# Performance work log

Hardware: AMD Instinct MI355X
Metric: run time of the kernel (lower is better)

Reference implementation:

```python
import jax, jax.numpy as jnp
import numpy as np

LEVELS = 32
RANGE = 1.0


def fake_quantize(w, levels=LEVELS, r=RANGE):
    # clamp -> scale -> round (straight-through) -> unscale
    wc = jnp.clip(w, -r, r)
    scale = (levels - 1) / (2 * r)
    ws = (wc + r) * scale
    wr = jax.lax.stop_gradient(jnp.round(ws) - ws) + ws  # STE round
    return wr / scale - r


def analog_linear(x, w, b):
    return x @ fake_quantize(w).T + b


def rnn_layer(x_seq, w_ih, w_hh, b_ih, b_hh):
    # x_seq: [B, T, I]; returns [B, T, H]. Plain tanh RNN, h0 = 0.
    B = x_seq.shape[0]
    H = w_hh.shape[0]
    # precompute input contribution once (memory-bound GEMM outside the scan)
    pre = jnp.einsum('bti,hi->bth', x_seq, w_ih) + b_ih + b_hh  # [B,T,H]
    pre_t = jnp.swapaxes(pre, 0, 1)  # [T,B,H]

    def step(h, p):
        h_new = jnp.tanh(p + h @ w_hh.T)
        return h_new, h_new

    h0 = jnp.zeros((B, H), dtype=x_seq.dtype)
    _, hs = jax.lax.scan(step, h0, pre_t)
    return jnp.swapaxes(hs, 0, 1)  # [B,T,H]


def setup_inputs() -> dict:
    key = jax.random.key(0)
    ks = jax.random.split(key, 20)
    B, T, F = 32, 8192, 10
    H, L = 256, 3
    CTX = F - 1  # 9
    RNN_IN = 1 + 32  # 33

    def init(k, shape, fan_in):
        bound = 1.0 / np.sqrt(fan_in)
        return jax.random.uniform(k, shape, jnp.float32, -bound, bound)

    inp = {
        'x': jax.random.normal(ks[0], (B, T, F), jnp.float32),
        # context MLP: 9 -> 64 -> 32
        'W1': init(ks[1], (64, CTX), CTX), 'b1': init(ks[2], (64,), CTX),
        'W2': init(ks[3], (32, 64), 64), 'b2': init(ks[4], (32,), 64),
        # RNN layers
        'w_ih0': init(ks[5], (H, RNN_IN), H), 'w_hh0': init(ks[6], (H, H), H),
        'b_ih0': init(ks[7], (H,), H), 'b_hh0': init(ks[8], (H,), H),
        'w_ih1': init(ks[9], (H, H), H), 'w_hh1': init(ks[10], (H, H), H),
        'b_ih1': init(ks[11], (H,), H), 'b_hh1': init(ks[12], (H,), H),
        'w_ih2': init(ks[13], (H, H), H), 'w_hh2': init(ks[14], (H, H), H),
        'b_ih2': init(ks[15], (H,), H), 'b_hh2': init(ks[16], (H,), H),
        # head: 256 -> 128 -> 1
        'Wh1': init(ks[17], (128, H), H), 'bh1': jnp.zeros((128,), jnp.float32),
        'Wh2': init(ks[18], (1, 128), 128), 'bh2': jnp.zeros((1,), jnp.float32),
    }
    return inp


def reference(x, W1, b1, W2, b2,
              w_ih0, w_hh0, b_ih0, b_hh0,
              w_ih1, w_hh1, b_ih1, b_hh1,
              w_ih2, w_hh2, b_ih2, b_hh2,
              Wh1, bh1, Wh2, bh2):
    # Eval-mode forward (no weight noise, no dropout); quantization always on.
    audio = x[:, :, 0:1]              # [B,T,1]
    raw_ctx = x[:, 0, 1:]             # [B,9]
    h = jax.nn.relu(analog_linear(raw_ctx, W1, b1))
    ctx_emb = jnp.tanh(analog_linear(h, W2, b2))  # [B,32]
    T = audio.shape[1]
    ctx_exp = jnp.broadcast_to(ctx_emb[:, None, :], (x.shape[0], T, 32))
    rnn_in = jnp.concatenate([audio, ctx_exp], axis=2)  # [B,T,33]

    out = rnn_layer(rnn_in, w_ih0, w_hh0, b_ih0, b_hh0)
    out = rnn_layer(out, w_ih1, w_hh1, b_ih1, b_hh1)
    out = rnn_layer(out, w_ih2, w_hh2, b_ih2, b_hh2)

    y = jax.nn.gelu(analog_linear(out, Wh1, bh1), approximate=False)
    y = analog_linear(y, Wh2, bh2)    # [B,T,1]
    return y
```

## Files before the change

kernel.cpp:

```cpp
#include <hip/hip_runtime.h>
#include <cstdint>
#include <cstddef>

#define TT 8192
#define BB 32
#define HH 256
#define TC 512
#define NCH 16
#define NSLOT (NCH + 2)
#define CROWS (BB * TC)

__device__ __forceinline__ float qz(float x){
  float wc = fminf(fmaxf(x, -1.f), 1.f);
  return rintf((wc + 1.f) * 15.5f) / 15.5f - 1.f;
}

__device__ __forceinline__ float ftanh(float s){
  float sc = fminf(fmaxf(s, -15.f), 15.f);
  float e = __expf(2.f * sc);
  return (e - 1.f) * __builtin_amdgcn_rcpf(e + 1.f);
}

#define DPPADD(v, ctrl) \
  (v) += __int_as_float(__builtin_amdgcn_update_dpp(0, __float_as_int(v), (ctrl), 0xF, 0xF, true))

__global__ void quant_all(
  const float* __restrict__ W1, const float* __restrict__ W2,
  const float* __restrict__ Wh1, const float* __restrict__ Wh2,
  const float* __restrict__ bih1, const float* __restrict__ bhh1,
  const float* __restrict__ bih2, const float* __restrict__ bhh2,
  float* qW1, float* qW2, float* qWh1, float* qWh2,
  float* bL1, float* bL2)
{
  int i = blockIdx.x * 256 + threadIdx.x;
  if (i < 576){ qW1[i] = qz(W1[i]); return; }   i -= 576;
  if (i < 2048){ qW2[i] = qz(W2[i]); return; }  i -= 2048;
  if (i < 32768){ qWh1[i] = qz(Wh1[i]); return; } i -= 32768;
  if (i < 128){ qWh2[i] = qz(Wh2[i]); return; }  i -= 128;
  if (i < 256){ bL1[i] = bih1[i] + bhh1[i]; return; } i -= 256;
  if (i < 256){ bL2[i] = bih2[i] + bhh2[i]; return; }
}

__global__ void ctx_kernel(const float* __restrict__ x, const float* __restrict__ qW1,
  const float* __restrict__ b1, const float* __restrict__ qW2, const float* __restrict__ b2,
  const float* __restrict__ wih0, const float* __restrict__ bih0, const float* __restrict__ bhh0,
  float* __restrict__ cvec)
{
  __shared__ float rc[32][9];
  __shared__ float h1[32][64];
  __shared__ float ce[32][32];
  int tid = threadIdx.x;
  for (int i = tid; i < 288; i += 256){
    int b = i / 9, j = i % 9;
    rc[b][j] = x[(size_t)b * TT * 10 + 1 + j];
  }
  __syncthreads();
  for (int i = tid; i < 2048; i += 256){
    int b = i >> 6, o = i & 63;
    float s = b1[o];
    #pragma unroll
    for (int j = 0; j < 9; ++j) s = fmaf(rc[b][j], qW1[o*9 + j], s);
    h1[b][o] = fmaxf(s, 0.f);
  }
  __syncthreads();
  for (int i = tid; i < 1024; i += 256){
    int b = i >> 5, o = i & 31;
    float s = b2[o];
    #pragma unroll
    for (int j = 0; j < 64; ++j) s = fmaf(h1[b][j], qW2[o*64 + j], s);
    ce[b][o] = tanhf(s);
  }
  __syncthreads();
  for (int i = tid; i < 8192; i += 256){
    int b = i >> 8, o = i & 255;
    float s = bih0[o] + bhh0[o];
    #pragma unroll
    for (int j = 0; j < 32; ++j) s = fmaf(ce[b][j], wih0[o*33 + 1 + j], s);
    cvec[i] = s;
  }
}

__global__ __launch_bounds__(512, 2) void scan3(
  const float* __restrict__ whh0, const float* __restrict__ whh1, const float* __restrict__ whh2,
  const float* __restrict__ pre1, const float* __restrict__ pre2,
  const float* __restrict__ x, const float* __restrict__ cvec, const float* __restrict__ wih0,
  float* __restrict__ out0, float* __restrict__ out1, float* __restrict__ out2,
  float* __restrict__ hst0, float* __restrict__ hst1, float* __restrict__ hst2,
  int slot)
{
  __shared__ float hbuf[2][HH];
  const int layer = blockIdx.x >> 5;
  const int b = blockIdx.x & 31;
  const int c = slot - layer;
  if (c < 0 || c >= NCH) return;

  const float* whh = (layer == 0) ? whh0 : (layer == 1) ? whh1 : whh2;
  const float* pre = (layer == 1) ? pre1 : pre2;
  float* out = (layer == 0) ? out0 : (layer == 1) ? out1 : out2;
  float* hst = (layer == 0) ? hst0 : (layer == 1) ? hst1 : hst2;
  const int t0 = c * TC;

  const int tid = threadIdx.x;
  const int og = tid >> 4;
  const int kc = tid & 15;
  const int jm = kc & 7;
  const int o_mine = og * 8 + jm;

  float w[8][16];
  {
    const float* wr = whh + (size_t)(og * 8) * HH + kc * 16;
    #pragma unroll
    for (int j = 0; j < 8; ++j){
      #pragma unroll
      for (int m = 0; m < 4; ++m){
        float4 v = *(const float4*)(wr + (size_t)j * HH + m*4);
        w[j][m*4+0] = v.x; w[j][m*4+1] = v.y; w[j][m*4+2] = v.z; w[j][m*4+3] = v.w;
      }
    }
  }

  if (tid < HH){
    hbuf[0][tid] = (c == 0) ? 0.f : hst[(size_t)b * HH + tid];
  }

  float w0c = 0.f, cv = 0.f, pre_c;
  if (layer == 0){
    w0c = wih0[o_mine * 33];
    cv  = cvec[(size_t)b * HH + o_mine];
    pre_c = x[((size_t)b * TT + t0) * 10] * w0c + cv;
  } else {
    pre_c = pre[(size_t)(b * TC) * HH + o_mine];
  }
  __syncthreads();

  float hn = 0.f;
  for (int tl = 0; tl < TC; ++tl){
    #pragma unroll
    for (int j = 0; j < 8; ++j){
      asm volatile("" :
        "+v"(w[j][0]),  "+v"(w[j][1]),  "+v"(w[j][2]),  "+v"(w[j][3]),
        "+v"(w[j][4]),  "+v"(w[j][5]),  "+v"(w[j][6]),  "+v"(w[j][7]),
        "+v"(w[j][8]),  "+v"(w[j][9]),  "+v"(w[j][10]), "+v"(w[j][11]),
        "+v"(w[j][12]), "+v"(w[j][13]), "+v"(w[j][14]), "+v"(w[j][15]));
    }

    int tn = (tl + 1 < TC) ? (tl + 1) : tl;
    float pre_n;
    if (layer == 0){
      pre_n = x[((size_t)b * TT + t0 + tn) * 10] * w0c + cv;
    } else {
      pre_n = pre[(size_t)(b * TC + tn) * HH + o_mine];
    }

    float hv[16];
    {
      const float* hb = hbuf[tl & 1] + kc * 16;
      #pragma unroll
      for (int m = 0; m < 4; ++m){
        float4 v = *(const float4*)(hb + m*4);
        hv[m*4+0] = v.x; hv[m*4+1] = v.y; hv[m*4+2] = v.z; hv[m*4+3] = v.w;
      }
    }

    float acc[8];
    #pragma unroll
    for (int j = 0; j < 8; ++j){
      float s0 = 0.f, s1 = 0.f, s2 = 0.f, s3 = 0.f;
      #pragma unroll
      for (int m = 0; m < 4; ++m){
        s0 = fmaf(w[j][m*4+0], hv[m*4+0], s0);
        s1 = fmaf(w[j][m*4+1], hv[m*4+1], s1);
        s2 = fmaf(w[j][m*4+2], hv[m*4+2], s2);
        s3 = fmaf(w[j][m*4+3], hv[m*4+3], s3);
      }
      acc[j] = (s0 + s1) + (s2 + s3);
    }

    #pragma unroll
    for (int j = 0; j < 8; ++j){
      float v = acc[j];
      DPPADD(v, 0xB1);
      DPPADD(v, 0x4E);
      DPPADD(v, 0x124);
      DPPADD(v, 0x128);
      acc[j] = v;
    }

    float s = acc[0];
    s = (jm == 1) ? acc[1] : s;
    s = (jm == 2) ? acc[2] : s;
    s = (jm == 3) ? acc[3] : s;
    s = (jm == 4) ? acc[4] : s;
    s = (jm == 5) ? acc[5] : s;
    s = (jm == 6) ? acc[6] : s;
    s = (jm == 7) ? acc[7] : s;
    s += pre_c;
    hn = ftanh(s);
    if (kc < 8){
      hbuf[(tl & 1) ^ 1][o_mine] = hn;
      out[(size_t)(b * TC + tl) * HH + o_mine] = hn;
    }
    pre_c = pre_n;
    __syncthreads();
  }
  if (kc < 8) hst[(size_t)b * HH + o_mine] = hn;
}

__device__ __forceinline__ void gemm_tile(
  const float* __restrict__ A, const float* __restrict__ Bw,
  const float* __restrict__ bias, float* __restrict__ C,
  int bx, int by)
{
  __shared__ float As[16][132];
  __shared__ float Bs[16][132];
  const int tid = threadIdx.x;
  const int tx = tid & 15, ty = tid >> 4;
  const size_t n0 = (size_t)bx * 128;
  const int c0 = by * 128;
  float acc[8][8];
  #pragma unroll
  for (int i = 0; i < 8; ++i)
    #pragma unroll
    for (int j = 0; j < 8; ++j) acc[i][j] = 0.f;

  for (int k0 = 0; k0 < 256; k0 += 16){
    #pragma unroll
    for (int q = 0; q < 2; ++q){
      int f = tid + q*256;
      int row = f >> 2, k4 = f & 3;
      float4 va = *(const float4*)(A + (n0 + row)*256 + k0 + k4*4);
      As[k4*4+0][row] = va.x; As[k4*4+1][row] = va.y; As[k4*4+2][row] = va.z; As[k4*4+3][row] = va.w;
      float4 vb = *(const float4*)(Bw + (size_t)(c0 + row)*256 + k0 + k4*4);
      Bs[k4*4+0][row] = vb.x; Bs[k4*4+1][row] = vb.y; Bs[k4*4+2][row] = vb.z; Bs[k4*4+3][row] = vb.w;
    }
    __syncthreads();
    #pragma unroll
    for (int k = 0; k < 16; ++k){
      float a[8], bb[8];
      *(float4*)&a[0]  = *(const float4*)&As[k][ty*4];
      *(float4*)&a[4]  = *(const float4*)&As[k][ty*4 + 64];
      *(float4*)&bb[0] = *(const float4*)&Bs[k][tx*4];
      *(float4*)&bb[4] = *(const float4*)&Bs[k][tx*4 + 64];
      #pragma unroll
      for (int i = 0; i < 8; ++i)
        #pragma unroll
        for (int j = 0; j < 8; ++j) acc[i][j] = fmaf(a[i], bb[j], acc[i][j]);
    }
    __syncthreads();
  }
  #pragma unroll
  for (int i = 0; i < 8; ++i){
    size_t row = n0 + (size_t)ty*4 + (i & 3) + (i >> 2)*64;
    #pragma unroll
    for (int jh = 0; jh < 2; ++jh){
      int col = c0 + tx*4 + jh*64;
      float4 v;
      v.x = acc[i][jh*4+0] + bias[col+0];
      v.y = acc[i][jh*4+1] + bias[col+1];
      v.z = acc[i][jh*4+2] + bias[col+2];
      v.w = acc[i][jh*4+3] + bias[col+3];
      *(float4*)(C + row * 256 + col) = v;
    }
  }
}

__device__ __forceinline__ void head_tile(
  const float* __restrict__ A, const float* __restrict__ Bw,
  const float* __restrict__ bh1, const float* __restrict__ w2,
  const float* __restrict__ bh2, float* __restrict__ y,
  int bx, int c2)
{
  __shared__ float As[16][132];
  __shared__ float Bs[16][132];
  const int tid = threadIdx.x;
  const int tx = tid & 15, ty = tid >> 4;
  const size_t n0 = (size_t)bx * 128;
  float acc[8][8];
  #pragma unroll
  for (int i = 0; i < 8; ++i)
    #pragma unroll
    for (int j = 0; j < 8; ++j) acc[i][j] = 0.f;

  for (int k0 = 0; k0 < 256; k0 += 16){
    #pragma unroll
    for (int q = 0; q < 2; ++q){
      int f = tid + q*256;
      int row = f >> 2, k4 = f & 3;
      float4 va = *(const float4*)(A + (n0 + row)*256 + k0 + k4*4);
      As[k4*4+0][row] = va.x; As[k4*4+1][row] = va.y; As[k4*4+2][row] = va.z; As[k4*4+3][row] = va.w;
      float4 vb = *(const float4*)(Bw + (size_t)row*256 + k0 + k4*4);
      Bs[k4*4+0][row] = vb.x; Bs[k4*4+1][row] = vb.y; Bs[k4*4+2][row] = vb.z; Bs[k4*4+3][row] = vb.w;
    }
    __syncthreads();
    #pragma unroll
    for (int k = 0; k < 16; ++k){
      float a[8], bb[8];
      *(float4*)&a[0]  = *(const float4*)&As[k][ty*4];
      *(float4*)&a[4]  = *(const float4*)&As[k][ty*4 + 64];
      *(float4*)&bb[0] = *(const float4*)&Bs[k][tx*4];
      *(float4*)&bb[4] = *(const float4*)&Bs[k][tx*4 + 64];
      #pragma unroll
      for (int i = 0; i < 8; ++i)
        #pragma unroll
        for (int j = 0; j < 8; ++j) acc[i][j] = fmaf(a[i], bb[j], acc[i][j]);
    }
    __syncthreads();
  }
  float4 w2a = *(const float4*)(w2 + tx*4);
  float4 w2b = *(const float4*)(w2 + tx*4 + 64);
  const float bias2 = bh2[0];
  #pragma unroll
  for (int i = 0; i < 8; ++i){
    float p = 0.f;
    #pragma unroll
    for (int j = 0; j < 4; ++j){
      float g0 = acc[i][j]   + bh1[tx*4 + j];
      float g1 = acc[i][4+j] + bh1[tx*4 + 64 + j];
      g0 = 0.5f * g0 * (1.f + erff(g0 * 0.70710678118654752f));
      g1 = 0.5f * g1 * (1.f + erff(g1 * 0.70710678118654752f));
      p = fmaf(g0, ((const float*)&w2a)[j], p);
      p = fmaf(g1, ((const float*)&w2b)[j], p);
    }
    p += __int_as_float(__builtin_amdgcn_update_dpp(0, __float_as_int(p), 0x111, 0xF, 0xF, true));
    p += __int_as_float(__builtin_amdgcn_update_dpp(0, __float_as_int(p), 0x112, 0xF, 0xF, true));
    p += __int_as_float(__builtin_amdgcn_update_dpp(0, __float_as_int(p), 0x114, 0xF, 0xF, true));
    p += __int_as_float(__builtin_amdgcn_update_dpp(0, __float_as_int(p), 0x118, 0xF, 0xF, true));
    if (tx == 15){
      size_t n = n0 + (size_t)ty*4 + (i & 3) + (i >> 2)*64;
      int bsm = (int)(n >> 9);
      int tl  = (int)(n & (TC - 1));
      y[(size_t)bsm * TT + c2 * TC + tl] = p + bias2;
    }
  }
}

__global__ __launch_bounds__(256) void aux_kernel(
  const float* __restrict__ out0, const float* __restrict__ out1, const float* __restrict__ out2,
  const float* __restrict__ wih1, const float* __restrict__ bL1, float* __restrict__ pre1,
  const float* __restrict__ wih2, const float* __restrict__ bL2, float* __restrict__ pre2,
  const float* __restrict__ qWh1, const float* __restrict__ bh1,
  const float* __restrict__ qWh2, const float* __restrict__ bh2,
  float* __restrict__ y, int slot)
{
  const int bid = blockIdx.x;
  if (bid < 512){
    int sec = bid >> 8;
    int c = slot - sec;
    if (c < 0 || c >= NCH) return;
    int t = bid & 255;
    if (sec == 0) gemm_tile(out0, wih1, bL1, pre1, t >> 1, t & 1);
    else          gemm_tile(out1, wih2, bL2, pre2, t >> 1, t & 1);
  } else {
    int c2 = slot - 2;
    if (c2 < 0 || c2 >= NCH) return;
    head_tile(out2, qWh1, bh1, qWh2, bh2, y, bid - 512, c2);
  }
}

extern "C" void kernel_launch(void* const* d_in, const int* in_sizes, int n_in,
                              void* d_out, int out_size, void* d_ws, size_t ws_size,
                              hipStream_t stream)
{
  const float* x    = (const float*)d_in[0];
  const float* W1   = (const float*)d_in[1];
  const float* b1   = (const float*)d_in[2];
  const float* W2   = (const float*)d_in[3];
  const float* b2   = (const float*)d_in[4];
  const float* wih0 = (const float*)d_in[5];
  const float* whh0 = (const float*)d_in[6];
  const float* bih0 = (const float*)d_in[7];
  const float* bhh0 = (const float*)d_in[8];
  const float* wih1 = (const float*)d_in[9];
  const float* whh1 = (const float*)d_in[10];
  const float* bih1 = (const float*)d_in[11];
  const float* bhh1 = (const float*)d_in[12];
  const float* wih2 = (const float*)d_in[13];
  const float* whh2 = (const float*)d_in[14];
  const float* bih2 = (const float*)d_in[15];
  const float* bhh2 = (const float*)d_in[16];
  const float* Wh1  = (const float*)d_in[17];
  const float* bh1  = (const float*)d_in[18];
  const float* Wh2  = (const float*)d_in[19];
  const float* bh2  = (const float*)d_in[20];
  float* y = (float*)d_out;
  (void)in_sizes; (void)n_in; (void)out_size; (void)ws_size;

  char* p = (char*)d_ws;
  auto alloc = [&](size_t nfloats) -> float* {
    float* r = (float*)p;
    p += ((nfloats * sizeof(float) + 255) & ~(size_t)255);
    return r;
  };
  float* qW1  = alloc(576);
  float* qW2  = alloc(2048);
  float* qWh1 = alloc(32768);
  float* qWh2 = alloc(128);
  float* bL1  = alloc(256);
  float* bL2  = alloc(256);
  float* cvec = alloc((size_t)BB * HH);
  float* hst0 = alloc((size_t)BB * HH);
  float* hst1 = alloc((size_t)BB * HH);
  float* hst2 = alloc((size_t)BB * HH);
  float* out0 = alloc((size_t)CROWS * HH);
  float* out1 = alloc((size_t)CROWS * HH);
  float* out2 = alloc((size_t)CROWS * HH);
  float* pre1 = alloc((size_t)CROWS * HH);
  float* pre2 = alloc((size_t)CROWS * HH);

  quant_all<<<141, 256, 0, stream>>>(W1, W2, Wh1, Wh2,
                                     bih1, bhh1, bih2, bhh2,
                                     qW1, qW2, qWh1, qWh2, bL1, bL2);
  ctx_kernel<<<1, 256, 0, stream>>>(x, qW1, b1, qW2, b2, wih0, bih0, bhh0, cvec);

  for (int s = 0; s < NSLOT; ++s){
    scan3<<<96, 512, 0, stream>>>(whh0, whh1, whh2, pre1, pre2, x, cvec, wih0,
                                  out0, out1, out2, hst0, hst1, hst2, s);
    aux_kernel<<<640, 256, 0, stream>>>(out0, out1, out2,
                                        wih1, bL1, pre1,
                                        wih2, bL2, pre2,
                                        qWh1, bh1, qWh2, bh2, y, s);
  }
}
```

Before: 9.459 ms.

## Double scan block threads to 1024 with 4 rows per group and swizzled LDS h-buffer

```diff
diff --git a/kernel.cpp b/kernel.cpp
--- a/kernel.cpp
+++ b/kernel.cpp
@@ -24,6 +24,12 @@
 #define DPPADD(v, ctrl) \
   (v) += __int_as_float(__builtin_amdgcn_update_dpp(0, __float_as_int(v), (ctrl), 0xF, 0xF, true))
 
+__device__ __forceinline__ int swz(int o){
+  int g = o >> 2;
+  int gs = g ^ (g >> 3);
+  return gs * 4 + (o & 3);
+}
+
 __global__ void quant_all(
   const float* __restrict__ W1, const float* __restrict__ W2,
   const float* __restrict__ Wh1, const float* __restrict__ Wh2,
@@ -80,7 +86,7 @@
   }
 }
 
-__global__ __launch_bounds__(512, 2) void scan3(
+__global__ __attribute__((amdgpu_waves_per_eu(4, 4))) __launch_bounds__(1024) void scan3(
   const float* __restrict__ whh0, const float* __restrict__ whh1, const float* __restrict__ whh2,
   const float* __restrict__ pre1, const float* __restrict__ pre2,
   const float* __restrict__ x, const float* __restrict__ cvec, const float* __restrict__ wih0,
@@ -88,7 +94,8 @@
   float* __restrict__ hst0, float* __restrict__ hst1, float* __restrict__ hst2,
   int slot)
 {
-  __shared__ float hbuf[2][HH];
+  __shared__ float4 hb4[128];
+  float* hbuf = (float*)hb4;
   const int layer = blockIdx.x >> 5;
   const int b = blockIdx.x & 31;
   const int c = slot - layer;
@@ -103,24 +110,40 @@
   const int tid = threadIdx.x;
   const int og = tid >> 4;
   const int kc = tid & 15;
-  const int jm = kc & 7;
-  const int o_mine = og * 8 + jm;
-
-  float w[8][16];
+  const int jm = kc & 3;
+  const int o_mine = og * 4 + jm;
+
+  float w[4][16];
   {
-    const float* wr = whh + (size_t)(og * 8) * HH + kc * 16;
-    #pragma unroll
-    for (int j = 0; j < 8; ++j){
+    const float* wr = whh + (size_t)(og * 4) * HH + (kc << 4);
+    #pragma unroll
+    for (int j = 0; j < 4; ++j){
       #pragma unroll
       for (int m = 0; m < 4; ++m){
-        float4 v = *(const float4*)(wr + (size_t)j * HH + m*4);
+        float4 v = *(const float4*)(wr + (size_t)j * HH + m * 4);
         w[j][m*4+0] = v.x; w[j][m*4+1] = v.y; w[j][m*4+2] = v.z; w[j][m*4+3] = v.w;
       }
     }
   }
+  #pragma unroll
+  for (int j = 0; j < 4; ++j){
+    asm volatile("" :
+      "+v"(w[j][0]),  "+v"(w[j][1]),  "+v"(w[j][2]),  "+v"(w[j][3]),
+      "+v"(w[j][4]),  "+v"(w[j][5]),  "+v"(w[j][6]),  "+v"(w[j][7]),
+      "+v"(w[j][8]),  "+v"(w[j][9]),  "+v"(w[j][10]), "+v"(w[j][11]),
+      "+v"(w[j][12]), "+v"(w[j][13]), "+v"(w[j][14]), "+v"(w[j][15]));
+  }
+
+  int rdw[4];
+  #pragma unroll
+  for (int m = 0; m < 4; ++m){
+    int q = kc * 4 + m;
+    rdw[m] = (q ^ (q >> 3)) * 4;
+  }
+  const int wrw = swz(o_mine);
 
   if (tid < HH){
-    hbuf[0][tid] = (c == 0) ? 0.f : hst[(size_t)b * HH + tid];
+    hbuf[swz(tid)] = (c == 0) ? 0.f : hst[(size_t)b * HH + tid];
   }
 
   float w0c = 0.f, cv = 0.f, pre_c;
@@ -135,15 +158,6 @@
 
   float hn = 0.f;
   for (int tl = 0; tl < TC; ++tl){
-    #pragma unroll
-    for (int j = 0; j < 8; ++j){
-      asm volatile("" :
-        "+v"(w[j][0]),  "+v"(w[j][1]),  "+v"(w[j][2]),  "+v"(w[j][3]),
-        "+v"(w[j][4]),  "+v"(w[j][5]),  "+v"(w[j][6]),  "+v"(w[j][7]),
-        "+v"(w[j][8]),  "+v"(w[j][9]),  "+v"(w[j][10]), "+v"(w[j][11]),
-        "+v"(w[j][12]), "+v"(w[j][13]), "+v"(w[j][14]), "+v"(w[j][15]));
-    }
-
     int tn = (tl + 1 < TC) ? (tl + 1) : tl;
     float pre_n;
     if (layer == 0){
@@ -152,32 +166,28 @@
       pre_n = pre[(size_t)(b * TC + tn) * HH + o_mine];
     }
 
-    float hv[16];
-    {
-      const float* hb = hbuf[tl & 1] + kc * 16;
+    const int rbase = (tl & 1) << 8;
+    float4 hv[4];
+    #pragma unroll
+    for (int m = 0; m < 4; ++m)
+      hv[m] = *(const float4*)&hbuf[rbase + rdw[m]];
+
+    float acc[4];
+    #pragma unroll
+    for (int j = 0; j < 4; ++j){
+      float a0 = 0.f, a1 = 0.f, a2 = 0.f, a3 = 0.f;
       #pragma unroll
       for (int m = 0; m < 4; ++m){
-        float4 v = *(const float4*)(hb + m*4);
-        hv[m*4+0] = v.x; hv[m*4+1] = v.y; hv[m*4+2] = v.z; hv[m*4+3] = v.w;
+        a0 = fmaf(w[j][m*4+0], hv[m].x, a0);
+        a1 = fmaf(w[j][m*4+1], hv[m].y, a1);
+        a2 = fmaf(w[j][m*4+2], hv[m].z, a2);
+        a3 = fmaf(w[j][m*4+3], hv[m].w, a3);
       }
-    }
-
-    float acc[8];
-    #pragma unroll
-    for (int j = 0; j < 8; ++j){
-      float s0 = 0.f, s1 = 0.f, s2 = 0.f, s3 = 0.f;
-      #pragma unroll
-      for (int m = 0; m < 4; ++m){
-        s0 = fmaf(w[j][m*4+0], hv[m*4+0], s0);
-        s1 = fmaf(w[j][m*4+1], hv[m*4+1], s1);
-        s2 = fmaf(w[j][m*4+2], hv[m*4+2], s2);
-        s3 = fmaf(w[j][m*4+3], hv[m*4+3], s3);
-      }
-      acc[j] = (s0 + s1) + (s2 + s3);
-    }
-
-    #pragma unroll
-    for (int j = 0; j < 8; ++j){
+      acc[j] = (a0 + a1) + (a2 + a3);
+    }
+
+    #pragma unroll
+    for (int j = 0; j < 4; ++j){
       float v = acc[j];
       DPPADD(v, 0xB1);
       DPPADD(v, 0x4E);
@@ -190,20 +200,16 @@
     s = (jm == 1) ? acc[1] : s;
     s = (jm == 2) ? acc[2] : s;
     s = (jm == 3) ? acc[3] : s;
-    s = (jm == 4) ? acc[4] : s;
-    s = (jm == 5) ? acc[5] : s;
-    s = (jm == 6) ? acc[6] : s;
-    s = (jm == 7) ? acc[7] : s;
     s += pre_c;
     hn = ftanh(s);
-    if (kc < 8){
-      hbuf[(tl & 1) ^ 1][o_mine] = hn;
+    if (kc < 4){
+      hbuf[(((tl & 1) ^ 1) << 8) + wrw] = hn;
       out[(size_t)(b * TC + tl) * HH + o_mine] = hn;
     }
     pre_c = pre_n;
     __syncthreads();
   }
-  if (kc < 8) hst[(size_t)b * HH + o_mine] = hn;
+  if (kc < 4) hst[(size_t)b * HH + o_mine] = hn;
 }
 
 __device__ __forceinline__ void gemm_tile(
@@ -413,8 +419,8 @@
   ctx_kernel<<<1, 256, 0, stream>>>(x, qW1, b1, qW2, b2, wih0, bih0, bhh0, cvec);
 
   for (int s = 0; s < NSLOT; ++s){
-    scan3<<<96, 512, 0, stream>>>(whh0, whh1, whh2, pre1, pre2, x, cvec, wih0,
-                                  out0, out1, out2, hst0, hst1, hst2, s);
+    scan3<<<96, 1024, 0, stream>>>(whh0, whh1, whh2, pre1, pre2, x, cvec, wih0,
+                                   out0, out1, out2, hst0, hst1, hst2, s);
     aux_kernel<<<640, 256, 0, stream>>>(out0, out1, out2,
                                         wih1, bL1, pre1,
                                         wih2, bL2, pre2,
```

Measured after the change: 8.852 ms. 6.4% less time.
